# Kernel tuning notes

Hardware: AMD Instinct MI355X
Metric: run time of the kernel (lower is better)

The kernel has to match this reference:

```python
import jax, jax.numpy as jnp
import numpy as np

B, T, L, H = 16, 16, 512, 768


def setup_inputs() -> dict:
    key = jax.random.key(0)
    k1, k2, k3, k4, k5, k6 = jax.random.split(key, 6)
    hn = jax.random.normal(k1, (B, L, H), dtype=jnp.float32)
    decoder_out = jax.random.normal(k2, (B, L, H), dtype=jnp.float32)
    W1 = jax.random.normal(k3, (H, H), dtype=jnp.float32) * (1.0 / np.sqrt(H))
    W2 = jax.random.normal(k4, (H, H), dtype=jnp.float32) * (1.0 / np.sqrt(H))
    V = jax.random.normal(k5, (H,), dtype=jnp.float32) * (1.0 / np.sqrt(H))
    # Ragged, consistent pointer indices: T monotone segment starts per sample,
    # gold boundary Yindex[b,t] in [Xindex[b,t], L).
    step = L // T  # 32
    Xindex = jnp.broadcast_to(jnp.arange(T, dtype=jnp.int64) * step, (B, T))
    offsets = jax.random.randint(k6, (B, T), 0, step, dtype=jnp.int64)
    Yindex = Xindex + offsets
    lens = jnp.full((B,), L, dtype=jnp.int64)
    return {"hn": hn, "decoder_out": decoder_out, "W1": W1, "W2": W2, "V": V,
            "Xindex": Xindex, "Yindex": Yindex, "lens": lens}


def reference(hn, decoder_out, W1, W2, V, Xindex, Yindex, lens):
    # Faithful batched form of training_decoder + pointerLayer:
    #   for each sample i, step j:
    #     en = hn[i, Xindex[i,j]:lens[i]]            (ragged suffix)
    #     dj = decoder_out[i, Yindex[i,j]]           (cur_dj = decoder_out[cur_groundy])
    #     s  = selu(V @ selu(W1 en + W2 dj))
    #     loss += NLL(log_softmax(s), Yindex[i,j]-Xindex[i,j])
    WE = jnp.einsum('blh,gh->blg', hn, W1)                        # [B,L,H]  nnW1(en)
    dj = jnp.take_along_axis(decoder_out, Yindex[:, :, None], axis=1)  # [B,T,H]
    WD = jnp.einsum('bth,gh->btg', dj, W2)                        # [B,T,H]  nnW2(dj)
    act = jax.nn.selu(WE[:, None, :, :] + WD[:, :, None, :])      # [B,T,L,H]
    scores = jax.nn.selu(jnp.einsum('btlh,h->btl', act, V))       # [B,T,L]
    pos = jnp.arange(hn.shape[1])
    mask = (pos[None, None, :] >= Xindex[:, :, None]) & (pos[None, None, :] < lens[:, None, None])
    neg_inf = jnp.finfo(scores.dtype).min
    masked = jnp.where(mask, scores, neg_inf)
    logp = masked - jax.scipy.special.logsumexp(masked, axis=-1, keepdims=True)
    # logits index (Yindex - Xindex) in the sliced array == global index Yindex
    gold = jnp.take_along_axis(logp, Yindex[:, :, None], axis=-1)[..., 0]  # [B,T]
    return -jnp.mean(gold)
```

## Files before the change

kernel.cpp:

```cpp
#include <hip/hip_runtime.h>
#include <hip/hip_bf16.h>
#include <math.h>

#define SELU_SCALE 1.0507009873554805f
#define SELU_ALPHA 1.6732632423543772f

static constexpr int B_ = 16, T_ = 16, L_ = 512, H_ = 768;

typedef __bf16 bf16x8 __attribute__((ext_vector_type(8)));
typedef float  f32x4  __attribute__((ext_vector_type(4)));

__device__ __forceinline__ float bf_lo(unsigned u) { return __uint_as_float(u << 16); }
__device__ __forceinline__ float bf_hi(unsigned u) { return __uint_as_float(u & 0xFFFF0000u); }

__device__ __forceinline__ float selu_core(float x) {
    float e = fmaf(__expf(x), SELU_ALPHA, -SELU_ALPHA);
    return x > 0.0f ? x : e;
}

__device__ __forceinline__ int xsw(int r) { return (r >> 1) & 3; }

__device__ __forceinline__ bf16x8 pack8(float4 a, float4 b) {
    bf16x8 o;
    o[0] = (__bf16)a.x; o[1] = (__bf16)a.y; o[2] = (__bf16)a.z; o[3] = (__bf16)a.w;
    o[4] = (__bf16)b.x; o[5] = (__bf16)b.y; o[6] = (__bf16)b.z; o[7] = (__bf16)b.w;
    return o;
}

__global__ __launch_bounds__(256, 2) void gemm_k(
        const float* __restrict__ hn, const float* __restrict__ dec,
        const float* __restrict__ w1, const float* __restrict__ w2,
        const int* __restrict__ Yi,
        __bf16* __restrict__ web, float* __restrict__ wdf,
        float* __restrict__ out) {
    __shared__ __bf16 As[128 * 32];
    __shared__ __bf16 Bs[128 * 32];

    const int tid = threadIdx.x;
    if (blockIdx.x == 0 && tid == 0) out[0] = 0.0f;

    int bx = blockIdx.x;
    const float* Wf; int m0, n0; bool wd;
    if (bx < 384) {
        wd = false; Wf = w1;
        m0 = (bx & 63) * 128; n0 = (bx >> 6) * 128;
    } else {
        wd = true; bx -= 384; Wf = w2;
        m0 = (bx & 1) * 128;  n0 = (bx >> 1) * 128;
    }

    const int wave = tid >> 6, lane = tid & 63;
    const int wm = (wave >> 1) * 64, wn = (wave & 1) * 64;
    const int lr = lane & 15, q = lane >> 4;

    const int r1 = wave * 32 + (lane >> 2);
    const int s3 = lane & 3;
    const int g1 = s3 ^ xsw(r1);

    const float *aG1, *aG2;
    if (!wd) {
        aG1 = hn + (size_t)(m0 + r1) * 768 + g1 * 8;
        aG2 = aG1 + (size_t)16 * 768;
    } else {
        int bt1 = m0 + r1, bt2 = bt1 + 16;
        aG1 = dec + ((size_t)((bt1 >> 4) * L_ + Yi[bt1])) * 768 + g1 * 8;
        aG2 = dec + ((size_t)((bt2 >> 4) * L_ + Yi[bt2])) * 768 + g1 * 8;
    }
    const float* bG1 = Wf + (size_t)(n0 + r1) * 768 + g1 * 8;
    const float* bG2 = bG1 + (size_t)16 * 768;

    bf16x8* AsW1 = (bf16x8*)&As[r1 * 32 + s3 * 8];
    bf16x8* AsW2 = (bf16x8*)&As[(r1 + 16) * 32 + s3 * 8];
    bf16x8* BsW1 = (bf16x8*)&Bs[r1 * 32 + s3 * 8];
    bf16x8* BsW2 = (bf16x8*)&Bs[(r1 + 16) * 32 + s3 * 8];

    int aoff[4], boff[4];
#pragma unroll
    for (int i = 0; i < 4; ++i) {
        int r = wm + i * 16 + lr;
        aoff[i] = r * 32 + (q ^ xsw(r)) * 8;
    }
#pragma unroll
    for (int j = 0; j < 4; ++j) {
        int r = wn + j * 16 + lr;
        boff[j] = r * 32 + (q ^ xsw(r)) * 8;
    }

    f32x4 acc[4][4] = {};

    float4 xa1a = *(const float4*)(aG1);      float4 xa1b = *(const float4*)(aG1 + 4);
    float4 xa2a = *(const float4*)(aG2);      float4 xa2b = *(const float4*)(aG2 + 4);
    float4 xb1a = *(const float4*)(bG1);      float4 xb1b = *(const float4*)(bG1 + 4);
    float4 xb2a = *(const float4*)(bG2);      float4 xb2b = *(const float4*)(bG2 + 4);
    float4 ya1a = *(const float4*)(aG1 + 32); float4 ya1b = *(const float4*)(aG1 + 36);
    float4 ya2a = *(const float4*)(aG2 + 32); float4 ya2b = *(const float4*)(aG2 + 36);
    float4 yb1a = *(const float4*)(bG1 + 32); float4 yb1b = *(const float4*)(bG1 + 36);
    float4 yb2a = *(const float4*)(bG2 + 32); float4 yb2b = *(const float4*)(bG2 + 36);

#pragma unroll 1
    for (int k0 = 0; k0 < 768; k0 += 64) {
        {
            *AsW1 = pack8(xa1a, xa1b);
            *AsW2 = pack8(xa2a, xa2b);
            *BsW1 = pack8(xb1a, xb1b);
            *BsW2 = pack8(xb2a, xb2b);
            asm volatile("s_waitcnt lgkmcnt(0)\n\ts_barrier" ::: "memory");
            if (k0 + 64 < 768) {
                xa1a = *(const float4*)(aG1 + k0 + 64); xa1b = *(const float4*)(aG1 + k0 + 68);
                xa2a = *(const float4*)(aG2 + k0 + 64); xa2b = *(const float4*)(aG2 + k0 + 68);
                xb1a = *(const float4*)(bG1 + k0 + 64); xb1b = *(const float4*)(bG1 + k0 + 68);
                xb2a = *(const float4*)(bG2 + k0 + 64); xb2b = *(const float4*)(bG2 + k0 + 68);
            }
            bf16x8 af[4], bfr[4];
#pragma unroll
            for (int i = 0; i < 4; ++i) af[i]  = *(const bf16x8*)&As[aoff[i]];
#pragma unroll
            for (int j = 0; j < 4; ++j) bfr[j] = *(const bf16x8*)&Bs[boff[j]];
#pragma unroll
            for (int i = 0; i < 4; ++i)
#pragma unroll
                for (int j = 0; j < 4; ++j)
                    acc[i][j] = __builtin_amdgcn_mfma_f32_16x16x32_bf16(af[i], bfr[j], acc[i][j], 0, 0, 0);
            asm volatile("s_barrier" ::: "memory");
        }
        {
            *AsW1 = pack8(ya1a, ya1b);
            *AsW2 = pack8(ya2a, ya2b);
            *BsW1 = pack8(yb1a, yb1b);
            *BsW2 = pack8(yb2a, yb2b);
            asm volatile("s_waitcnt lgkmcnt(0)\n\ts_barrier" ::: "memory");
            if (k0 + 96 < 768) {
                ya1a = *(const float4*)(aG1 + k0 + 96); ya1b = *(const float4*)(aG1 + k0 + 100);
                ya2a = *(const float4*)(aG2 + k0 + 96); ya2b = *(const float4*)(aG2 + k0 + 100);
                yb1a = *(const float4*)(bG1 + k0 + 96); yb1b = *(const float4*)(bG1 + k0 + 100);
                yb2a = *(const float4*)(bG2 + k0 + 96); yb2b = *(const float4*)(bG2 + k0 + 100);
            }
            bf16x8 af[4], bfr[4];
#pragma unroll
            for (int i = 0; i < 4; ++i) af[i]  = *(const bf16x8*)&As[aoff[i]];
#pragma unroll
            for (int j = 0; j < 4; ++j) bfr[j] = *(const bf16x8*)&Bs[boff[j]];
#pragma unroll
            for (int i = 0; i < 4; ++i)
#pragma unroll
                for (int j = 0; j < 4; ++j)
                    acc[i][j] = __builtin_amdgcn_mfma_f32_16x16x32_bf16(af[i], bfr[j], acc[i][j], 0, 0, 0);
            asm volatile("s_barrier" ::: "memory");
        }
    }

#pragma unroll
    for (int i = 0; i < 4; ++i)
#pragma unroll
        for (int j = 0; j < 4; ++j)
#pragma unroll
            for (int r = 0; r < 4; ++r) {
                int row = m0 + wm + i * 16 + q * 4 + r;
                int col = n0 + wn + j * 16 + lr;
                if (!wd) web[(size_t)row * 768 + col] = (__bf16)acc[i][j][r];
                else     wdf[(size_t)row * 768 + col] = acc[i][j][r];
            }
}

__global__ __launch_bounds__(256) void scores_k(
        const __bf16* __restrict__ web, const float* __restrict__ wdf,
        const float* __restrict__ V, const int* __restrict__ Xi,
        float* __restrict__ scores) {
    const int b  = blockIdx.x;
    const int l0 = ((int)gridDim.y - 1 - (int)blockIdx.y) * 16;
    const int tid = threadIdx.x;
    const int ls = tid >> 4, hc = tid & 15;
    const int l  = l0 + ls;
    const int h0 = hc * 8;

    float we[48], vv[48];
    const __bf16* wr = web + ((size_t)(b * L_ + l)) * H_ + h0;
#pragma unroll
    for (int j = 0; j < 6; ++j) {
        uint4 u = *(const uint4*)(wr + j * 128);
        we[j*8+0] = bf_lo(u.x); we[j*8+1] = bf_hi(u.x);
        we[j*8+2] = bf_lo(u.y); we[j*8+3] = bf_hi(u.y);
        we[j*8+4] = bf_lo(u.z); we[j*8+5] = bf_hi(u.z);
        we[j*8+6] = bf_lo(u.w); we[j*8+7] = bf_hi(u.w);
    }
    const float* vp = V + h0;
#pragma unroll
    for (int j = 0; j < 6; ++j) {
        float4 a = *(const float4*)(vp + j * 128);
        float4 c = *(const float4*)(vp + j * 128 + 4);
        vv[j*8+0] = a.x; vv[j*8+1] = a.y; vv[j*8+2] = a.z; vv[j*8+3] = a.w;
        vv[j*8+4] = c.x; vv[j*8+5] = c.y; vv[j*8+6] = c.z; vv[j*8+7] = c.w;
    }

    const int wmaxl = l0 + ((tid >> 6) << 2) + 3;
    const int bT = b * T_;
#pragma unroll 1
    for (int t = 0; t < T_; ++t) {
        const int X = Xi[bT + t];
        if (wmaxl < X) continue;
        const float* wdp = wdf + ((size_t)(bT + t)) * H_ + h0;
        float a0 = 0.f, a1 = 0.f, a2 = 0.f, a3 = 0.f;
#pragma unroll
        for (int j = 0; j < 6; ++j) {
            float4 x = *(const float4*)(wdp + j * 128);
            float4 y = *(const float4*)(wdp + j * 128 + 4);
            a0 = fmaf(selu_core(we[j*8+0] + x.x), vv[j*8+0], a0);
            a1 = fmaf(selu_core(we[j*8+1] + x.y), vv[j*8+1], a1);
            a2 = fmaf(selu_core(we[j*8+2] + x.z), vv[j*8+2], a2);
            a3 = fmaf(selu_core(we[j*8+3] + x.w), vv[j*8+3], a3);
            a0 = fmaf(selu_core(we[j*8+4] + y.x), vv[j*8+4], a0);
            a1 = fmaf(selu_core(we[j*8+5] + y.y), vv[j*8+5], a1);
            a2 = fmaf(selu_core(we[j*8+6] + y.z), vv[j*8+6], a2);
            a3 = fmaf(selu_core(we[j*8+7] + y.w), vv[j*8+7], a3);
        }
        float dot = (a0 + a1) + (a2 + a3);
        dot += __shfl_xor(dot, 1);
        dot += __shfl_xor(dot, 2);
        dot += __shfl_xor(dot, 4);
        dot += __shfl_xor(dot, 8);
        if (hc == 0) {
            dot *= SELU_SCALE;
            float sc = dot > 0.0f ? SELU_SCALE * dot
                                  : SELU_SCALE * SELU_ALPHA * (__expf(dot) - 1.0f);
            scores[((size_t)(bT + t)) * L_ + l] = sc;
        }
    }
}

__global__ __launch_bounds__(64) void loss_k(
        const float* __restrict__ scores, const int* __restrict__ Xi,
        const int* __restrict__ Yi, float* __restrict__ out) {
    const int bt = blockIdx.x;
    const int lane = threadIdx.x;
    const int X = Xi[bt];
    const int Y = Yi[bt];
    const float* row = scores + (size_t)bt * L_;

    float m = -INFINITY;
    for (int l = X + lane; l < L_; l += 64) m = fmaxf(m, row[l]);
#pragma unroll
    for (int off = 32; off > 0; off >>= 1) m = fmaxf(m, __shfl_xor(m, off));

    float s = 0.0f;
    for (int l = X + lane; l < L_; l += 64) s += __expf(row[l] - m);
#pragma unroll
    for (int off = 32; off > 0; off >>= 1) s += __shfl_xor(s, off);

    if (lane == 0)
        atomicAdd(out, (m + __logf(s) - row[Y]) * (1.0f / (B_ * T_)));
}

extern "C" void kernel_launch(void* const* d_in, const int* in_sizes, int n_in,
                              void* d_out, int out_size, void* d_ws, size_t ws_size,
                              hipStream_t stream) {
    const float* hn  = (const float*)d_in[0];
    const float* dec = (const float*)d_in[1];
    const float* W1  = (const float*)d_in[2];
    const float* W2  = (const float*)d_in[3];
    const float* V   = (const float*)d_in[4];
    const int*   Xi  = (const int*)d_in[5];
    const int*   Yi  = (const int*)d_in[6];
    float* out = (float*)d_out;

    char* ws = (char*)d_ws;
    size_t off = 0;
    auto alloc = [&](size_t bytes) -> char* {
        char* p = ws + off;
        off += (bytes + 255) & ~(size_t)255;
        return p;
    };
    __bf16* web    = (__bf16*)alloc((size_t)B_ * L_ * H_ * 2);
    float*  wdf    = (float*)alloc((size_t)B_ * T_ * H_ * 4);
    float*  scores = (float*)alloc((size_t)B_ * T_ * L_ * 4);

    gemm_k<<<396, 256, 0, stream>>>(hn, dec, W1, W2, Yi, web, wdf, out);
    scores_k<<<dim3(B_, L_ / 16), 256, 0, stream>>>(web, wdf, V, Xi, scores);
    loss_k<<<B_ * T_, 64, 0, stream>>>(scores, Xi, Yi, out);
}
```

Before: 166.7 us.

## Pre-convert weights to bf16 and load B fragments directly; split scores over T

Measured after the change: 161.8 us. 2.9% less time.

```diff
diff --git a/kernel.cpp b/kernel.cpp
--- a/kernel.cpp
+++ b/kernel.cpp
@@ -6,6 +6,7 @@
 #define SELU_ALPHA 1.6732632423543772f
 
 static constexpr int B_ = 16, T_ = 16, L_ = 512, H_ = 768;
+static constexpr int WSZ = 768 * 768;
 
 typedef __bf16 bf16x8 __attribute__((ext_vector_type(8)));
 typedef float  f32x4  __attribute__((ext_vector_type(4)));
@@ -27,25 +28,32 @@
     return o;
 }
 
+__global__ __launch_bounds__(256) void prep_k(
+        const float* __restrict__ w1, const float* __restrict__ w2,
+        __bf16* __restrict__ wb, float* __restrict__ out) {
+    if (blockIdx.x == 0 && threadIdx.x == 0) out[0] = 0.0f;
+    int idx = (blockIdx.x * 256 + threadIdx.x) * 8;
+    const float* src = idx < WSZ ? w1 + idx : w2 + (idx - WSZ);
+    float4 a = *(const float4*)src;
+    float4 b = *(const float4*)(src + 4);
+    *(bf16x8*)(wb + idx) = pack8(a, b);
+}
+
 __global__ __launch_bounds__(256, 2) void gemm_k(
         const float* __restrict__ hn, const float* __restrict__ dec,
-        const float* __restrict__ w1, const float* __restrict__ w2,
-        const int* __restrict__ Yi,
-        __bf16* __restrict__ web, float* __restrict__ wdf,
-        float* __restrict__ out) {
+        const __bf16* __restrict__ wb, const int* __restrict__ Yi,
+        __bf16* __restrict__ web, float* __restrict__ wdf) {
     __shared__ __bf16 As[128 * 32];
-    __shared__ __bf16 Bs[128 * 32];
 
     const int tid = threadIdx.x;
-    if (blockIdx.x == 0 && tid == 0) out[0] = 0.0f;
 
     int bx = blockIdx.x;
-    const float* Wf; int m0, n0; bool wd;
+    const __bf16* Wb; int m0, n0; bool wd;
     if (bx < 384) {
-        wd = false; Wf = w1;
+        wd = false; Wb = wb;
         m0 = (bx & 63) * 128; n0 = (bx >> 6) * 128;
     } else {
-        wd = true; bx -= 384; Wf = w2;
+        wd = true; bx -= 384; Wb = wb + WSZ;
         m0 = (bx & 1) * 128;  n0 = (bx >> 1) * 128;
     }
 
@@ -66,85 +74,74 @@
         aG1 = dec + ((size_t)((bt1 >> 4) * L_ + Yi[bt1])) * 768 + g1 * 8;
         aG2 = dec + ((size_t)((bt2 >> 4) * L_ + Yi[bt2])) * 768 + g1 * 8;
     }
-    const float* bG1 = Wf + (size_t)(n0 + r1) * 768 + g1 * 8;
-    const float* bG2 = bG1 + (size_t)16 * 768;
 
     bf16x8* AsW1 = (bf16x8*)&As[r1 * 32 + s3 * 8];
     bf16x8* AsW2 = (bf16x8*)&As[(r1 + 16) * 32 + s3 * 8];
-    bf16x8* BsW1 = (bf16x8*)&Bs[r1 * 32 + s3 * 8];
-    bf16x8* BsW2 = (bf16x8*)&Bs[(r1 + 16) * 32 + s3 * 8];
-
-    int aoff[4], boff[4];
+
+    int aoff[4];
 #pragma unroll
     for (int i = 0; i < 4; ++i) {
         int r = wm + i * 16 + lr;
         aoff[i] = r * 32 + (q ^ xsw(r)) * 8;
     }
-#pragma unroll
-    for (int j = 0; j < 4; ++j) {
-        int r = wn + j * 16 + lr;
-        boff[j] = r * 32 + (q ^ xsw(r)) * 8;
-    }
+
+    const __bf16* pB = Wb + (size_t)(n0 + wn + lr) * 768 + q * 8;
 
     f32x4 acc[4][4] = {};
 
     float4 xa1a = *(const float4*)(aG1);      float4 xa1b = *(const float4*)(aG1 + 4);
     float4 xa2a = *(const float4*)(aG2);      float4 xa2b = *(const float4*)(aG2 + 4);
-    float4 xb1a = *(const float4*)(bG1);      float4 xb1b = *(const float4*)(bG1 + 4);
-    float4 xb2a = *(const float4*)(bG2);      float4 xb2b = *(const float4*)(bG2 + 4);
     float4 ya1a = *(const float4*)(aG1 + 32); float4 ya1b = *(const float4*)(aG1 + 36);
     float4 ya2a = *(const float4*)(aG2 + 32); float4 ya2b = *(const float4*)(aG2 + 36);
-    float4 yb1a = *(const float4*)(bG1 + 32); float4 yb1b = *(const float4*)(bG1 + 36);
-    float4 yb2a = *(const float4*)(bG2 + 32); float4 yb2b = *(const float4*)(bG2 + 36);
+
+    bf16x8 bX[4], bY[4];
+#pragma unroll
+    for (int j = 0; j < 4; ++j) bX[j] = *(const bf16x8*)(pB + j * 12288);
 
 #pragma unroll 1
     for (int k0 = 0; k0 < 768; k0 += 64) {
         {
             *AsW1 = pack8(xa1a, xa1b);
             *AsW2 = pack8(xa2a, xa2b);
-            *BsW1 = pack8(xb1a, xb1b);
-            *BsW2 = pack8(xb2a, xb2b);
             asm volatile("s_waitcnt lgkmcnt(0)\n\ts_barrier" ::: "memory");
             if (k0 + 64 < 768) {
                 xa1a = *(const float4*)(aG1 + k0 + 64); xa1b = *(const float4*)(aG1 + k0 + 68);
                 xa2a = *(const float4*)(aG2 + k0 + 64); xa2b = *(const float4*)(aG2 + k0 + 68);
-                xb1a = *(const float4*)(bG1 + k0 + 64); xb1b = *(const float4*)(bG1 + k0 + 68);
-                xb2a = *(const float4*)(bG2 + k0 + 64); xb2b = *(const float4*)(bG2 + k0 + 68);
-            }
-            bf16x8 af[4], bfr[4];
-#pragma unroll
-            for (int i = 0; i < 4; ++i) af[i]  = *(const bf16x8*)&As[aoff[i]];
-#pragma unroll
-            for (int j = 0; j < 4; ++j) bfr[j] = *(const bf16x8*)&Bs[boff[j]];
+            }
+#pragma unroll
+            for (int j = 0; j < 4; ++j)
+                bY[j] = *(const bf16x8*)(pB + j * 12288 + k0 + 32);
+            bf16x8 af[4];
+#pragma unroll
+            for (int i = 0; i < 4; ++i) af[i] = *(const bf16x8*)&As[aoff[i]];
 #pragma unroll
             for (int i = 0; i < 4; ++i)
 #pragma unroll
                 for (int j = 0; j < 4; ++j)
-                    acc[i][j] = __builtin_amdgcn_mfma_f32_16x16x32_bf16(af[i], bfr[j], acc[i][j], 0, 0, 0);
+                    acc[i][j] = __builtin_amdgcn_mfma_f32_16x16x32_bf16(af[i], bX[j], acc[i][j], 0, 0, 0);
             asm volatile("s_barrier" ::: "memory");
         }
         {
             *AsW1 = pack8(ya1a, ya1b);
             *AsW2 = pack8(ya2a, ya2b);
-            *BsW1 = pack8(yb1a, yb1b);
-            *BsW2 = pack8(yb2a, yb2b);
             asm volatile("s_waitcnt lgkmcnt(0)\n\ts_barrier" ::: "memory");
             if (k0 + 96 < 768) {
                 ya1a = *(const float4*)(aG1 + k0 + 96); ya1b = *(const float4*)(aG1 + k0 + 100);
                 ya2a = *(const float4*)(aG2 + k0 + 96); ya2b = *(const float4*)(aG2 + k0 + 100);
-                yb1a = *(const float4*)(bG1 + k0 + 96); yb1b = *(const float4*)(bG1 + k0 + 100);
-                yb2a = *(const float4*)(bG2 + k0 + 96); yb2b = *(const float4*)(bG2 + k0 + 100);
-            }
-            bf16x8 af[4], bfr[4];
-#pragma unroll
-            for (int i = 0; i < 4; ++i) af[i]  = *(const bf16x8*)&As[aoff[i]];
-#pragma unroll
-            for (int j = 0; j < 4; ++j) bfr[j] = *(const bf16x8*)&Bs[boff[j]];
+            }
+            if (k0 + 64 < 768) {
+#pragma unroll
+                for (int j = 0; j < 4; ++j)
+                    bX[j] = *(const bf16x8*)(pB + j * 12288 + k0 + 64);
+            }
+            bf16x8 af[4];
+#pragma unroll
+            for (int i = 0; i < 4; ++i) af[i] = *(const bf16x8*)&As[aoff[i]];
 #pragma unroll
             for (int i = 0; i < 4; ++i)
 #pragma unroll
                 for (int j = 0; j < 4; ++j)
-                    acc[i][j] = __builtin_amdgcn_mfma_f32_16x16x32_bf16(af[i], bfr[j], acc[i][j], 0, 0, 0);
+                    acc[i][j] = __builtin_amdgcn_mfma_f32_16x16x32_bf16(af[i], bY[j], acc[i][j], 0, 0, 0);
             asm volatile("s_barrier" ::: "memory");
         }
     }
@@ -162,12 +159,13 @@
             }
 }
 
-__global__ __launch_bounds__(256) void scores_k(
+__global__ __launch_bounds__(256, 4) void scores_k(
         const __bf16* __restrict__ web, const float* __restrict__ wdf,
         const float* __restrict__ V, const int* __restrict__ Xi,
         float* __restrict__ scores) {
     const int b  = blockIdx.x;
     const int l0 = ((int)gridDim.y - 1 - (int)blockIdx.y) * 16;
+    const int t0 = blockIdx.z * 8;
     const int tid = threadIdx.x;
     const int ls = tid >> 4, hc = tid & 15;
     const int l  = l0 + ls;
@@ -195,7 +193,7 @@
     const int wmaxl = l0 + ((tid >> 6) << 2) + 3;
     const int bT = b * T_;
 #pragma unroll 1
-    for (int t = 0; t < T_; ++t) {
+    for (int t = t0; t < t0 + 8; ++t) {
         const int X = Xi[bT + t];
         if (wmaxl < X) continue;
         const float* wdp = wdf + ((size_t)(bT + t)) * H_ + h0;
@@ -272,8 +270,10 @@
     __bf16* web    = (__bf16*)alloc((size_t)B_ * L_ * H_ * 2);
     float*  wdf    = (float*)alloc((size_t)B_ * T_ * H_ * 4);
     float*  scores = (float*)alloc((size_t)B_ * T_ * L_ * 4);
-
-    gemm_k<<<396, 256, 0, stream>>>(hn, dec, W1, W2, Yi, web, wdf, out);
-    scores_k<<<dim3(B_, L_ / 16), 256, 0, stream>>>(web, wdf, V, Xi, scores);
+    __bf16* wb     = (__bf16*)alloc((size_t)2 * WSZ * 2);
+
+    prep_k<<<2 * WSZ / (256 * 8), 256, 0, stream>>>(W1, W2, wb, out);
+    gemm_k<<<396, 256, 0, stream>>>(hn, dec, wb, Yi, web, wdf);
+    scores_k<<<dim3(B_, L_ / 16, 2), 256, 0, stream>>>(web, wdf, V, Xi, scores);
     loss_k<<<B_ * T_, 64, 0, stream>>>(scores, Xi, Yi, out);
 }
```
